# Optimization experiments

Measured on AMD Instinct MI355X. Metric: run time of the kernel, lower is better.

The kernel has to match this reference:

```python
import jax, jax.numpy as jnp
import numpy as np

B, FIN, H, W = 16, 256, 32, 32
NH, FH = 8, 64
CIN = FIN + 2  # fin + 2 coordinate-grid pos channels
COUT = NH * FH


def setup_inputs() -> dict:
    key = jax.random.key(0)
    ks = jax.random.split(key, 9)
    s = 1.0 / np.sqrt(CIN)
    so = 1.0 / np.sqrt(COUT)
    return {
        "x": jax.random.normal(ks[0], (B, FIN, H, W), dtype=jnp.float32),
        "wq": jax.random.uniform(ks[1], (COUT, CIN), jnp.float32, -s, s),
        "bq": jax.random.uniform(ks[2], (COUT,), jnp.float32, -s, s),
        "wk": jax.random.uniform(ks[3], (COUT, CIN), jnp.float32, -s, s),
        "bk": jax.random.uniform(ks[4], (COUT,), jnp.float32, -s, s),
        "wv": jax.random.uniform(ks[5], (COUT, CIN), jnp.float32, -s, s),
        "bv": jax.random.uniform(ks[6], (COUT,), jnp.float32, -s, s),
        "wo": jax.random.uniform(ks[7], (FIN, COUT), jnp.float32, -so, so),
        "bo": jax.random.uniform(ks[8], (FIN,), jnp.float32, -so, so),
    }


def reference(x, wq, bq, wk, bk, wv, bv, wo, bo):
    b, c, h, w = x.shape
    n = h * w
    # PosEncoding: concat one linspace(-1,1) coordinate channel per spatial dim
    gy, gx = jnp.meshgrid(jnp.linspace(-1.0, 1.0, h), jnp.linspace(-1.0, 1.0, w), indexing="ij")
    pos = jnp.broadcast_to(jnp.stack([gy, gx])[None], (b, 2, h, w)).astype(x.dtype)
    t = jnp.concatenate([x, pos], axis=1).reshape(b, c + 2, n)  # [B, C+2, N]
    # 1x1 convs are per-token GEMMs
    q = (jnp.einsum("oc,bcn->bon", wq, t) + bq[:, None]).reshape(b, NH, FH, n)
    k = (jnp.einsum("oc,bcn->bon", wk, t) + bk[:, None]).reshape(b, NH, FH, n)
    v = (jnp.einsum("oc,bcn->bon", wv, t) + bv[:, None]).reshape(b, NH, FH, n)
    temp = FH ** 0.5
    attn = jax.nn.softmax(jnp.einsum("bhdn,bhdm->bhnm", q, k) / temp, axis=-1)
    o = jnp.einsum("bhnm,bhdm->bhdn", attn, v).reshape(b, NH * FH, n)
    o = jnp.einsum("oc,bcn->bon", wo, o) + bo[:, None]
    return x + o.reshape(b, c, h, w)
```

## Files before the change

### kernel.cpp

```cpp
#include <hip/hip_runtime.h>


typedef unsigned short u16;
typedef unsigned int   u32;
typedef __attribute__((ext_vector_type(8))) short  short8;
typedef __attribute__((ext_vector_type(4))) float  float4_;

#define MFMA16(a, b, c) __builtin_amdgcn_mfma_f32_16x16x32_bf16(a, b, c, 0, 0, 0)
#define GLOAD_LDS16(g, l) \
    __builtin_amdgcn_global_load_lds((const __attribute__((address_space(1))) void*)(g), \
                                     (__attribute__((address_space(3))) void*)(l), 16, 0, 0)

__device__ __forceinline__ float bf2f(u16 u) {
    union { u32 i; float f; } v; v.i = ((u32)u) << 16; return v.f;
}
__device__ __forceinline__ u16 f2bf(float f) {
    union { float f; u32 i; } v; v.f = f;
    u32 r = v.i + 0x7FFFu + ((v.i >> 16) & 1u);
    return (u16)(r >> 16);
}
__device__ __forceinline__ float exp2_fast(float x) {
    float r;
    asm("v_exp_f32 %0, %1" : "=v"(r) : "v"(x));
    return r;
}
__device__ __forceinline__ u32 cvtpk_bf16(float lo, float hi) {
    u32 r;
    asm("v_cvt_pk_bf16_f32 %0, %1, %2" : "=v"(r) : "v"(lo), "v"(hi));
    return r;
}
__device__ __forceinline__ void pl32swap(u32 &x, u32 &y) {
    asm volatile("v_permlane32_swap_b32 %0, %1" : "+v"(x), "+v"(y));
}
__device__ __forceinline__ void pl16swap(u32 &x, u32 &y) {
    asm volatile("v_permlane16_swap_b32 %0, %1" : "+v"(x), "+v"(y));
}

__global__ __launch_bounds__(256) void prep(
    const float* __restrict__ wq, const float* __restrict__ wk,
    const float* __restrict__ wv, const float* __restrict__ x,
    u16* __restrict__ wb, u16* __restrict__ xT)
{
    __shared__ float Lt[64][65];
    const int bid = blockIdx.x;
    const int tid = threadIdx.x;
    if (bid < 512) {
        int i = bid * 256 + tid;
        int o = i >> 8, c = i & 255;
        size_t si = (size_t)o * 258 + c;
        wb[i]          = f2bf(wq[si]);
        wb[131072 + i] = f2bf(wk[si]);
        wb[262144 + i] = f2bf(wv[si]);
    } else {
        int r = bid - 512;
        int n0 = (r & 15) * 64, c0 = ((r >> 4) & 3) * 64, b = r >> 6;
#pragma unroll
        for (int p = 0; p < 4; ++p) {
            int c = p * 16 + (tid >> 4);
            int nn = (tid & 15) * 4;
            float4 v = *(const float4*)&x[((size_t)(b * 256) + c0 + c) * 1024 + n0 + nn];
            Lt[c][nn + 0] = v.x; Lt[c][nn + 1] = v.y;
            Lt[c][nn + 2] = v.z; Lt[c][nn + 3] = v.w;
        }
        __syncthreads();
#pragma unroll
        for (int p = 0; p < 4; ++p) {
            int n = p * 16 + (tid >> 4);
            int cc = (tid & 15) * 4;
            ushort4 st;
            st.x = f2bf(Lt[cc + 0][n]); st.y = f2bf(Lt[cc + 1][n]);
            st.z = f2bf(Lt[cc + 2][n]); st.w = f2bf(Lt[cc + 3][n]);
            *(ushort4*)&xT[((size_t)(b << 10) + n0 + n) * 256 + c0 + cc] = st;
        }
    }
}

__global__ __launch_bounds__(512) void qkv_mfma(
    const u16* __restrict__ xT, const u16* __restrict__ wb,
    const float* __restrict__ wq, const float* __restrict__ wk,
    const float* __restrict__ wv,
    const float* __restrict__ bq, const float* __restrict__ bk,
    const float* __restrict__ bv,
    u16* __restrict__ qkvbuf)
{
    __shared__ __align__(1024) u16 Wl2[2][256 * 32];
    __shared__ __align__(1024) u16 Tl2[2][128 * 32];
    const int tid = threadIdx.x;
    const int lane = tid & 63, w = tid >> 6;
    const int quad = lane >> 4, m15 = lane & 15;
    const int n0 = blockIdx.x * 128, mt2 = blockIdx.y, b = blockIdx.z;
    const int mat = mt2 >> 1;
    const int m0 = mt2 * 256;
    const float* worig = (mat == 0) ? wq : ((mat == 1) ? wk : wv);
    const float* bias  = (mat == 0) ? bq : ((mat == 1) ? bk : bv);
    const float oscale = (mat == 1) ? 0.1803368801111204f : 1.0f;
    u16* outbuf = qkvbuf + (size_t)mat * 8388608;

    float4_ acc[2][8];
#pragma unroll
    for (int s = 0; s < 2; ++s)
#pragma unroll
        for (int t = 0; t < 8; ++t) acc[s][t] = (float4_){0, 0, 0, 0};

    const int lr2 = lane >> 2, li2 = lane & 3;
    const int wrow0 = (2 * w) * 16 + lr2;
    const int wrow1 = (2 * w + 1) * 16 + lr2;
    const int trow  = w * 16 + lr2;
    const int wc0 = (li2 ^ ((wrow0 >> 1) & 3)) * 8;
    const int wc1 = (li2 ^ ((wrow1 >> 1) & 3)) * 8;
    const int tc  = (li2 ^ ((trow  >> 1) & 3)) * 8;
    const u16* wsrc0 = wb + (size_t)(m0 + wrow0) * 256 + wc0;
    const u16* wsrc1 = wb + (size_t)(m0 + wrow1) * 256 + wc1;
    const u16* tsrc  = xT + ((size_t)(b << 10) + n0 + trow) * 256 + tc;

    const int sfr = (quad ^ ((m15 >> 1) & 3)) * 8;
    const int ra0 = (w * 32 + m15) * 32 + sfr;
    const int ra1 = (w * 32 + 16 + m15) * 32 + sfr;

    GLOAD_LDS16(wsrc0, &Wl2[0][(2 * w) * 512]);
    GLOAD_LDS16(wsrc1, &Wl2[0][(2 * w + 1) * 512]);
    GLOAD_LDS16(tsrc,  &Tl2[0][w * 512]);
    __syncthreads();

#pragma unroll
    for (int k = 0; k < 8; ++k) {
        const int p = k & 1;
        if (k < 7) {
            const int kc = (k + 1) * 32;
            GLOAD_LDS16(wsrc0 + kc, &Wl2[p ^ 1][(2 * w) * 512]);
            GLOAD_LDS16(wsrc1 + kc, &Wl2[p ^ 1][(2 * w + 1) * 512]);
            GLOAD_LDS16(tsrc + kc,  &Tl2[p ^ 1][w * 512]);
        }

        short8 af0 = *(const short8*)&Wl2[p][ra0];
        short8 af1 = *(const short8*)&Wl2[p][ra1];
        __builtin_amdgcn_s_setprio(1);
#pragma unroll
        for (int t = 0; t < 8; ++t) {
            short8 bf = *(const short8*)&Tl2[p][(t * 16 + m15) * 32 + sfr];
            acc[0][t] = MFMA16(af0, bf, acc[0][t]);
            acc[1][t] = MFMA16(af1, bf, acc[1][t]);
        }
        __builtin_amdgcn_s_setprio(0);

        __syncthreads();
    }

#pragma unroll
    for (int s = 0; s < 2; ++s) {
        const int om_base = (mt2 & 1) * 256 + w * 32 + s * 16;
        float wg[4], wx[4], bi[4];
#pragma unroll
        for (int r = 0; r < 4; ++r) {
            int om = om_base + quad * 4 + r;
            wg[r] = worig[(size_t)om * 258 + 256];
            wx[r] = worig[(size_t)om * 258 + 257];
            bi[r] = bias[om];
        }
        const int h = om_base >> 6;
        const int dbase = (om_base & 63) + quad * 4;
#pragma unroll
        for (int t = 0; t < 8; ++t) {
            int n = n0 + t * 16 + m15;
            float gy = -1.0f + 2.0f * (float)(n >> 5) / 31.0f;
            float gx = -1.0f + 2.0f * (float)(n & 31) / 31.0f;
            float v[4];
#pragma unroll
            for (int r = 0; r < 4; ++r)
                v[r] = (acc[s][t][r] + wg[r] * gy + wx[r] * gx + bi[r]) * oscale;
            if (mat != 2) {
                ushort4 st;
                st.x = f2bf(v[0]); st.y = f2bf(v[1]);
                st.z = f2bf(v[2]); st.w = f2bf(v[3]);
                *(ushort4*)&outbuf[((size_t)(b * 8 + h) * 1024 + n) * 64 + dbase] = st;
            } else {
#pragma unroll
                for (int r = 0; r < 4; ++r)
                    outbuf[((size_t)(b * 8 + h) * 64 + dbase + r) * 1024 + n] = f2bf(v[r]);
            }
        }
    }
}

__global__ __launch_bounds__(512) void attn_mfma(
    u16* __restrict__ qbuf, const u16* __restrict__ kbuf,
    const u16* __restrict__ vbuf)
{
    __shared__ u16 Kl[64 * 64];
    __shared__ u16 Vl[64 * 64];

    const int tid = threadIdx.x;
    const int lane = tid & 63, w = tid >> 6;
    const int quad = lane >> 4, m15 = lane & 15;
    const int bh = blockIdx.x;
    const int q0 = blockIdx.y * 256;
    u16* qb = qbuf + (size_t)bh * 65536;
    const u16* kb = kbuf + (size_t)bh * 65536;
    const u16* vb = vbuf + (size_t)bh * 65536;

    short8 qf[2][2];
#pragma unroll
    for (int s = 0; s < 2; ++s) {
        const u16* qr = qb + (size_t)(q0 + w * 32 + s * 16 + m15) * 64 + quad * 8;
        qf[s][0] = *(const short8*)qr;
        qf[s][1] = *(const short8*)(qr + 32);
    }

    float4_ O[2][4];
    float lp[2] = {0.0f, 0.0f};
#pragma unroll
    for (int s = 0; s < 2; ++s)
#pragma unroll
        for (int t = 0; t < 4; ++t) O[s][t] = (float4_){0, 0, 0, 0};

    const int row = tid >> 3, c8 = (tid & 7) * 8;
    const int stsw = c8 ^ ((row & 7) << 3);
    const int rdsw = (m15 & 7) << 3;

    for (int kt0 = 0; kt0 < 1024; kt0 += 64) {
        __syncthreads();
        *(short8*)&Kl[row * 64 + stsw] =
            *(const short8*)(kb + (size_t)(kt0 + row) * 64 + c8);
        *(short8*)&Vl[row * 64 + stsw] =
            *(const short8*)(vb + (size_t)row * 1024 + kt0 + c8);
        __syncthreads();

        float4_ S[2][4];
#pragma unroll
        for (int s = 0; s < 2; ++s)
#pragma unroll
            for (int t = 0; t < 4; ++t) S[s][t] = (float4_){0, 0, 0, 0};
#pragma unroll
        for (int c = 0; c < 2; ++c) {
            short8 kf[4];
#pragma unroll
            for (int t = 0; t < 4; ++t)
                kf[t] = *(const short8*)&Kl[(t * 16 + m15) * 64 +
                                            ((c * 32 + quad * 8) ^ rdsw)];
            __builtin_amdgcn_s_setprio(1);
#pragma unroll
            for (int s = 0; s < 2; ++s)
#pragma unroll
                for (int t = 0; t < 4; ++t)
                    S[s][t] = MFMA16(kf[t], qf[s][c], S[s][t]);
            __builtin_amdgcn_s_setprio(0);
        }

        u32 W0[2][4], W1[2][4];
#pragma unroll
        for (int s = 0; s < 2; ++s) {
            float lsum = 0.0f;
#pragma unroll
            for (int t = 0; t < 4; ++t) {
                float p0 = exp2_fast(S[s][t][0]);
                float p1 = exp2_fast(S[s][t][1]);
                float p2 = exp2_fast(S[s][t][2]);
                float p3 = exp2_fast(S[s][t][3]);
                W0[s][t] = cvtpk_bf16(p0, p1);
                W1[s][t] = cvtpk_bf16(p2, p3);
                lsum += (p0 + p1) + (p2 + p3);
            }
            lp[s] += lsum;
        }

#pragma unroll
        for (int c = 0; c < 2; ++c) {
            short8 av[4];
#pragma unroll
            for (int dt = 0; dt < 4; ++dt)
                av[dt] = *(const short8*)&Vl[(dt * 16 + m15) * 64 +
                                             ((c * 32 + quad * 8) ^ rdsw)];
#pragma unroll
            for (int s = 0; s < 2; ++s) {
                u32 a = W0[s][2 * c], d = W0[s][2 * c + 1];
                pl32swap(a, d); pl16swap(a, d);
                u32 bb = W1[s][2 * c], e = W1[s][2 * c + 1];
                pl32swap(bb, e); pl16swap(bb, e);
                union { u32 u[4]; short8 v; } bpu;
                bpu.u[0] = a; bpu.u[1] = bb; bpu.u[2] = d; bpu.u[3] = e;
                short8 bp = bpu.v;
                __builtin_amdgcn_s_setprio(1);
#pragma unroll
                for (int dt = 0; dt < 4; ++dt)
                    O[s][dt] = MFMA16(av[dt], bp, O[s][dt]);
                __builtin_amdgcn_s_setprio(0);
            }
        }
    }

#pragma unroll
    for (int s = 0; s < 2; ++s) {
        float v = lp[s];
        v += __shfl_xor(v, 16);
        v += __shfl_xor(v, 32);
        float linv = 1.0f / v;
        int n = q0 + w * 32 + s * 16 + m15;
#pragma unroll
        for (int dt = 0; dt < 4; ++dt) {
            ushort4 st;
            st.x = f2bf(O[s][dt][0] * linv);
            st.y = f2bf(O[s][dt][1] * linv);
            st.z = f2bf(O[s][dt][2] * linv);
            st.w = f2bf(O[s][dt][3] * linv);
            *(ushort4*)&qb[(size_t)n * 64 + dt * 16 + quad * 4] = st;
        }
    }
}

__global__ __launch_bounds__(256) void proj_mfma(
    const u16* __restrict__ ao, const float* __restrict__ wo,
    const float* __restrict__ bo, const float* __restrict__ x,
    float* __restrict__ out)
{
    __shared__ u16 Wl[64 * 64];
    __shared__ u16 Tl[64 * 64];
    const int tid = threadIdx.x;
    const int lane = tid & 63, w = tid >> 6;
    const int quad = lane >> 4, m15 = lane & 15;
    const int n0 = blockIdx.x * 64, f0 = blockIdx.y * 64, b = blockIdx.z;

    float4_ acc[4] = {{0,0,0,0},{0,0,0,0},{0,0,0,0},{0,0,0,0}};
    const int srow = tid >> 2;
    const int sc8  = (tid & 3) * 8;
    const int sw0  = (srow & 7) << 3;
    const int rdsw = (m15 & 7) << 3;

    const float* wsrc = wo + (size_t)(f0 + srow) * 512 + sc8;
    const u16* tbase = ao + ((size_t)(b << 3) * 1024 + n0 + srow) * 64 + sc8;

    {
        float4 v0 = *(const float4*)(wsrc);
        float4 v1 = *(const float4*)(wsrc + 4);
        uint4 pk;
        pk.x = cvtpk_bf16(v0.x, v0.y); pk.y = cvtpk_bf16(v0.z, v0.w);
        pk.z = cvtpk_bf16(v1.x, v1.y); pk.w = cvtpk_bf16(v1.z, v1.w);
        *(uint4*)&Wl[srow * 64 + (sc8 ^ sw0)] = pk;
        *(short8*)&Tl[srow * 64 + (sc8 ^ sw0)] = *(const short8*)(tbase);
    }
    __syncthreads();

#pragma unroll
    for (int k = 0; k < 16; ++k) {
        const int p = k & 1;
        float4 pv0, pv1; short8 pt;
        if (k < 15) {
            const int kc = (k + 1) * 32;
            pv0 = *(const float4*)(wsrc + kc);
            pv1 = *(const float4*)(wsrc + kc + 4);
            pt  = *(const short8*)(tbase + (size_t)(kc >> 6) * 65536 + (kc & 63));
        }

        const int cb = p * 32 + quad * 8;
        short8 af = *(const short8*)&Wl[(w * 16 + m15) * 64 + (cb ^ rdsw)];
        __builtin_amdgcn_s_setprio(1);
#pragma unroll
        for (int t = 0; t < 4; ++t) {
            short8 bf = *(const short8*)&Tl[(t * 16 + m15) * 64 + (cb ^ rdsw)];
            acc[t] = MFMA16(af, bf, acc[t]);
        }
        __builtin_amdgcn_s_setprio(0);

        if (k < 15) {
            const int pc = ((p ^ 1) * 32 + sc8) ^ sw0;
            uint4 pk;
            pk.x = cvtpk_bf16(pv0.x, pv0.y); pk.y = cvtpk_bf16(pv0.z, pv0.w);
            pk.z = cvtpk_bf16(pv1.x, pv1.y); pk.w = cvtpk_bf16(pv1.z, pv1.w);
            *(uint4*)&Wl[srow * 64 + pc] = pk;
            *(short8*)&Tl[srow * 64 + pc] = pt;
        }
        __syncthreads();
    }

    float bi[4];
#pragma unroll
    for (int r = 0; r < 4; ++r) bi[r] = bo[f0 + w * 16 + quad * 4 + r];
#pragma unroll
    for (int t = 0; t < 4; ++t) {
        int n = n0 + t * 16 + m15;
#pragma unroll
        for (int r = 0; r < 4; ++r) {
            int f = f0 + w * 16 + quad * 4 + r;
            size_t idx = ((size_t)(b * 256) + f) * 1024 + n;
            out[idx] = acc[t][r] + bi[r] + x[idx];
        }
    }
}

extern "C" void kernel_launch(void* const* d_in, const int* in_sizes, int n_in,
                              void* d_out, int out_size, void* d_ws, size_t ws_size,
                              hipStream_t stream) {
    const float* x  = (const float*)d_in[0];
    const float* wq = (const float*)d_in[1];
    const float* bq = (const float*)d_in[2];
    const float* wk = (const float*)d_in[3];
    const float* bk = (const float*)d_in[4];
    const float* wv = (const float*)d_in[5];
    const float* bv = (const float*)d_in[6];
    const float* wo = (const float*)d_in[7];
    const float* bo = (const float*)d_in[8];

    u16* qkvbuf = (u16*)d_ws;
    u16* region = qkvbuf + 3 * 8388608;
    u16* xT = region;
    u16* wb = region + 4194304;

    prep<<<1536, 256, 0, stream>>>(wq, wk, wv, x, wb, xT);

    qkv_mfma<<<dim3(8, 6, 16), 512, 0, stream>>>(
        xT, wb, wq, wk, wv, bq, bk, bv, qkvbuf);

    attn_mfma<<<dim3(128, 4), 512, 0, stream>>>(
        qkvbuf, qkvbuf + 8388608, qkvbuf + 16777216);

    proj_mfma<<<dim3(16, 4, 16), 256, 0, stream>>>(qkvbuf, wo, bo, x, (float*)d_out);
}
```

Baseline: 165.6 us.

## Software-pipeline attention loop: overlap QK/softmax of next tile with PV of current

Double-buffers the K and V LDS tiles and restructures the key loop so that the QK^T MFMA and exp for tile i+1 are issued next to the PV MFMA for tile i. This is meant to give the scheduler independent MFMA and exp work to interleave, hiding exp latency and the LDS reads. The setprio hints around the first GEMM are removed. In exchange it uses twice the LDS, needs extra registers for the second probability set, and still synchronises twice per tile.

After: 174.4 us. 5.3% more time.

```diff
diff --git a/kernel.cpp b/kernel.cpp
--- a/kernel.cpp
+++ b/kernel.cpp
@@ -186,8 +186,8 @@
     u16* __restrict__ qbuf, const u16* __restrict__ kbuf,
     const u16* __restrict__ vbuf)
 {
-    __shared__ u16 Kl[64 * 64];
-    __shared__ u16 Vl[64 * 64];
+    __shared__ u16 Ksh[2][64 * 64];
+    __shared__ u16 Vsh[2][64 * 64];
 
     const int tid = threadIdx.x;
     const int lane = tid & 63, w = tid >> 6;
@@ -217,14 +217,15 @@
     const int stsw = c8 ^ ((row & 7) << 3);
     const int rdsw = (m15 & 7) << 3;
 
-    for (int kt0 = 0; kt0 < 1024; kt0 += 64) {
-        __syncthreads();
-        *(short8*)&Kl[row * 64 + stsw] =
+    u32 Wa0[2][4], Wa1[2][4], Wn0[2][4], Wn1[2][4];
+
+    auto STAGE = [&](int buf, int kt0) {
+        *(short8*)&Ksh[buf][row * 64 + stsw] =
             *(const short8*)(kb + (size_t)(kt0 + row) * 64 + c8);
-        *(short8*)&Vl[row * 64 + stsw] =
+        *(short8*)&Vsh[buf][row * 64 + stsw] =
             *(const short8*)(vb + (size_t)row * 1024 + kt0 + c8);
-        __syncthreads();
-
+    };
+    auto GEMM1SM = [&](const u16* Kl, u32 (&A0)[2][4], u32 (&A1)[2][4]) {
         float4_ S[2][4];
 #pragma unroll
         for (int s = 0; s < 2; ++s)
@@ -237,16 +238,12 @@
             for (int t = 0; t < 4; ++t)
                 kf[t] = *(const short8*)&Kl[(t * 16 + m15) * 64 +
                                             ((c * 32 + quad * 8) ^ rdsw)];
-            __builtin_amdgcn_s_setprio(1);
 #pragma unroll
             for (int s = 0; s < 2; ++s)
 #pragma unroll
                 for (int t = 0; t < 4; ++t)
                     S[s][t] = MFMA16(kf[t], qf[s][c], S[s][t]);
-            __builtin_amdgcn_s_setprio(0);
-        }
-
-        u32 W0[2][4], W1[2][4];
+        }
 #pragma unroll
         for (int s = 0; s < 2; ++s) {
             float lsum = 0.0f;
@@ -256,13 +253,14 @@
                 float p1 = exp2_fast(S[s][t][1]);
                 float p2 = exp2_fast(S[s][t][2]);
                 float p3 = exp2_fast(S[s][t][3]);
-                W0[s][t] = cvtpk_bf16(p0, p1);
-                W1[s][t] = cvtpk_bf16(p2, p3);
+                A0[s][t] = cvtpk_bf16(p0, p1);
+                A1[s][t] = cvtpk_bf16(p2, p3);
                 lsum += (p0 + p1) + (p2 + p3);
             }
             lp[s] += lsum;
         }
-
+    };
+    auto GEMM2 = [&](const u16* Vl, u32 (&A0)[2][4], u32 (&A1)[2][4]) {
 #pragma unroll
         for (int c = 0; c < 2; ++c) {
             short8 av[4];
@@ -272,9 +270,9 @@
                                              ((c * 32 + quad * 8) ^ rdsw)];
 #pragma unroll
             for (int s = 0; s < 2; ++s) {
-                u32 a = W0[s][2 * c], d = W0[s][2 * c + 1];
+                u32 a = A0[s][2 * c], d = A0[s][2 * c + 1];
                 pl32swap(a, d); pl16swap(a, d);
-                u32 bb = W1[s][2 * c], e = W1[s][2 * c + 1];
+                u32 bb = A1[s][2 * c], e = A1[s][2 * c + 1];
                 pl32swap(bb, e); pl16swap(bb, e);
                 union { u32 u[4]; short8 v; } bpu;
                 bpu.u[0] = a; bpu.u[1] = bb; bpu.u[2] = d; bpu.u[3] = e;
@@ -286,7 +284,29 @@
                 __builtin_amdgcn_s_setprio(0);
             }
         }
-    }
+    };
+
+    STAGE(0, 0);
+    __syncthreads();
+    GEMM1SM(&Ksh[0][0], Wa0, Wa1);
+    STAGE(1, 64);
+    __syncthreads();
+
+    for (int it = 0; it < 14; it += 2) {
+        GEMM1SM(&Ksh[1][0], Wn0, Wn1);
+        GEMM2(&Vsh[0][0], Wa0, Wa1);
+        __syncthreads();
+        STAGE(0, (it + 2) * 64);
+        __syncthreads();
+        GEMM1SM(&Ksh[0][0], Wa0, Wa1);
+        GEMM2(&Vsh[1][0], Wn0, Wn1);
+        __syncthreads();
+        STAGE(1, (it + 3) * 64);
+        __syncthreads();
+    }
+    GEMM1SM(&Ksh[1][0], Wn0, Wn1);
+    GEMM2(&Vsh[0][0], Wa0, Wa1);
+    GEMM2(&Vsh[1][0], Wn0, Wn1);
 
 #pragma unroll
     for (int s = 0; s < 2; ++s) {
```
